# Kernel tuning notes

Measured on AMD Instinct MI355X. Metric: run time of the kernel, lower is better.

The kernel has to match this reference:

```python
import jax, jax.numpy as jnp
import numpy as np

ALPHA = 0.2   # LeakyReLU negative slope
NEG = -1e9    # mask value for non-edges


def setup_inputs() -> dict:
    key = jax.random.key(0)
    ks = jax.random.split(key, 8)
    N, Din, F, H, Dout = 4096, 512, 64, 8, 16
    adj = (jax.random.uniform(ks[0], (N, N)) < 0.01).astype(jnp.float32)
    adjacency = jnp.maximum(adj, jnp.eye(N, dtype=jnp.float32))
    X = jax.random.normal(ks[1], (N, Din), jnp.float32)
    s = lambda k, shape, fan: jax.random.normal(k, shape, jnp.float32) / np.float32(np.sqrt(fan))
    W = s(ks[2], (H, Din, F), Din)        # per-head projection, stacked
    a1 = s(ks[3], (H, F), F)              # attention vector, source half
    a2 = s(ks[4], (H, F), F)              # attention vector, target half
    Wo = s(ks[5], (H * F, Dout), H * F)   # output-layer projection
    ao1 = s(ks[6], (Dout,), Dout)
    ao2 = s(ks[7], (Dout,), Dout)
    return dict(adjacency=adjacency, X=X, W=W, a1=a1, a2=a2, Wo=Wo, ao1=ao1, ao2=ao2)


def reference(adjacency, X, W, a1, a2, Wo, ao1, ao2):
    # dropout is identity (eval mode / p=0)
    mask = adjacency > 0
    N = X.shape[0]
    # --- multi-head attention layers (concat=True -> ELU) ---
    Wh = jnp.einsum('nd,hdf->hnf', X, W)                      # [H, N, F]
    f1 = jnp.einsum('hnf,hf->hn', Wh, a1)                     # [H, N]
    f2 = jnp.einsum('hnf,hf->hn', Wh, a2)                     # [H, N]
    e = jax.nn.leaky_relu(f1[:, :, None] + f2[:, None, :], ALPHA)  # [H, N, N]
    att = jax.nn.softmax(jnp.where(mask[None], e, NEG), axis=-1)
    heads = jax.nn.elu(jnp.einsum('hnm,hmf->hnf', att, Wh))   # [H, N, F]
    cat = jnp.transpose(heads, (1, 0, 2)).reshape(N, -1)      # [N, H*F]
    # --- output attention layer (concat=False -> no ELU) ---
    Who = cat @ Wo                                            # [N, Dout]
    eo = jax.nn.leaky_relu((Who @ ao1)[:, None] + (Who @ ao2)[None, :], ALPHA)
    atto = jax.nn.softmax(jnp.where(mask, eo, NEG), axis=-1)  # [N, N]
    return atto @ Who                                         # [N, Dout]
```

## Files before the change

### kernel.cpp

```cpp
#include <hip/hip_runtime.h>
#include <hip/hip_bf16.h>

#define N_NODES 4096
#define DIN     512
#define FDIM    64
#define NHEADS  8
#define DOUT    16
#define MAXN    512

typedef __attribute__((ext_vector_type(8))) short bf16x8;
typedef __attribute__((ext_vector_type(4))) float f32x4;

static __device__ __forceinline__ float us2f(unsigned short u) {
    union { unsigned int i; float f; } cv; cv.i = ((unsigned int)u) << 16; return cv.f;
}
static __device__ __forceinline__ unsigned short f2us(float v) {
    __hip_bfloat16 b = __float2bfloat16(v);
    return *(const unsigned short*)&b;
}
static __device__ __forceinline__ int is_f32(const void* adj) {
    return (((const unsigned short*)adj)[0] == 0) ? 1 : 0;
}

__global__ __launch_bounds__(256) void prep_kernel(
    const void* __restrict__ adj, const void* __restrict__ W,
    const void* __restrict__ a1, const void* __restrict__ a2, const void* __restrict__ Wo,
    const void* __restrict__ ao1, const void* __restrict__ ao2,
    unsigned short* __restrict__ Wt, float* __restrict__ Woc,
    float* __restrict__ a1c, float* __restrict__ a2c,
    float* __restrict__ ao1c, float* __restrict__ ao2c)
{
    const int f32 = is_f32(adj);
    const int b = blockIdx.x;
    const int t = threadIdx.x;
    if (b < 64) {
        const int h  = b >> 3;
        const int d0 = (b & 7) * 64;
        __shared__ float tile[64][65];
        const size_t wbase = (size_t)h * DIN * FDIM + (size_t)d0 * FDIM;
#pragma unroll
        for (int pass = 0; pass < 16; ++pass) {
            int i = pass * 256 + t;
            int dl = i >> 6, f = i & 63;
            float v = f32 ? ((const float*)W)[wbase + dl * FDIM + f]
                          : us2f(((const unsigned short*)W)[wbase + dl * FDIM + f]);
            tile[dl][f] = v;
        }
        __syncthreads();
#pragma unroll
        for (int pass = 0; pass < 16; ++pass) {
            int i = pass * 256 + t;
            int f = i >> 6, dl = i & 63;
            Wt[((size_t)(h * FDIM + f)) * DIN + d0 + dl] = f2us(tile[dl][f]);
        }
        return;
    }
    const int i0 = (b - 64) * 256 + t;
    for (int i = i0; i < DIN * DOUT; i += 2048) {
        float v = f32 ? ((const float*)Wo)[i] : us2f(((const unsigned short*)Wo)[i]);
        Woc[i] = v;
    }
    if (i0 < 512) {
        a1c[i0] = f32 ? ((const float*)a1)[i0] : us2f(((const unsigned short*)a1)[i0]);
        a2c[i0] = f32 ? ((const float*)a2)[i0] : us2f(((const unsigned short*)a2)[i0]);
    }
    if (i0 < 16) {
        ao1c[i0] = f32 ? ((const float*)ao1)[i0] : us2f(((const unsigned short*)ao1)[i0]);
        ao2c[i0] = f32 ? ((const float*)ao2)[i0] : us2f(((const unsigned short*)ao2)[i0]);
    }
}

__global__ __launch_bounds__(256) void scan_wh_kernel(
    const void* __restrict__ adj, const void* __restrict__ X,
    const unsigned short* __restrict__ Wt,
    const float* __restrict__ a1c, const float* __restrict__ a2c,
    int* __restrict__ cnt, int* __restrict__ nbr,
    unsigned short* __restrict__ Whb, float* __restrict__ f1, float* __restrict__ f2)
{
    const int b   = blockIdx.x;
    const int tid = threadIdx.x;
    const int f32 = is_f32(adj);
    const int wv   = tid >> 6;
    const int lane = tid & 63;

    __shared__ float red[3][16][68];

    if (b < 1024) {
        const int n = b * 4 + wv;
        const unsigned long long lmask = (1ull << lane) - 1ull;
        int c = 0;
        int* nrow = nbr + (size_t)n * MAXN;
        if (f32) {
            const uint4* row = (const uint4*)((const unsigned int*)adj + (size_t)n * N_NODES);
#pragma unroll 4
            for (int it = 0; it < 16; ++it) {
                uint4 v = row[it * 64 + lane];
                int base = (it * 64 + lane) * 4;
                unsigned long long m0 = __ballot(v.x != 0u);
                unsigned long long m1 = __ballot(v.y != 0u);
                unsigned long long m2 = __ballot(v.z != 0u);
                unsigned long long m3 = __ballot(v.w != 0u);
                int p;
                p = c + __popcll(m0 & lmask); if (v.x && p < MAXN) nrow[p] = base + 0; c += __popcll(m0);
                p = c + __popcll(m1 & lmask); if (v.y && p < MAXN) nrow[p] = base + 1; c += __popcll(m1);
                p = c + __popcll(m2 & lmask); if (v.z && p < MAXN) nrow[p] = base + 2; c += __popcll(m2);
                p = c + __popcll(m3 & lmask); if (v.w && p < MAXN) nrow[p] = base + 3; c += __popcll(m3);
            }
        } else {
            const ushort4* row = (const ushort4*)((const unsigned short*)adj + (size_t)n * N_NODES);
#pragma unroll 4
            for (int it = 0; it < 16; ++it) {
                ushort4 v = row[it * 64 + lane];
                int base = (it * 64 + lane) * 4;
                unsigned long long m0 = __ballot(v.x != 0);
                unsigned long long m1 = __ballot(v.y != 0);
                unsigned long long m2 = __ballot(v.z != 0);
                unsigned long long m3 = __ballot(v.w != 0);
                int p;
                p = c + __popcll(m0 & lmask); if (v.x && p < MAXN) nrow[p] = base + 0; c += __popcll(m0);
                p = c + __popcll(m1 & lmask); if (v.y && p < MAXN) nrow[p] = base + 1; c += __popcll(m1);
                p = c + __popcll(m2 & lmask); if (v.z && p < MAXN) nrow[p] = base + 2; c += __popcll(m2);
                p = c + __popcll(m3 & lmask); if (v.w && p < MAXN) nrow[p] = base + 3; c += __popcll(m3);
            }
        }
        if (lane == 0) cnt[n] = (c < MAXN) ? c : MAXN;
        return;
    }

    const int tile = b - 1024;
    const int nt   = tile >> 3;
    const int h    = tile & 7;
    const int quad = lane >> 4;
    const int l16  = lane & 15;
    const int node = nt * 16 + l16;
    const int kbase = wv * 128 + quad * 8;

    f32x4 acc[4];
#pragma unroll
    for (int j = 0; j < 4; ++j) acc[j] = (f32x4){0.f, 0.f, 0.f, 0.f};

    const unsigned short* wp = Wt + (size_t)h * FDIM * DIN + kbase;
    if (f32) {
        const float* xp = (const float*)X + (size_t)node * DIN + kbase;
#pragma unroll
        for (int ks = 0; ks < 4; ++ks) {
            float4 xa = *(const float4*)(xp + ks * 32);
            float4 xb = *(const float4*)(xp + ks * 32 + 4);
            bf16x8 xf;
            xf[0] = (short)f2us(xa.x); xf[1] = (short)f2us(xa.y);
            xf[2] = (short)f2us(xa.z); xf[3] = (short)f2us(xa.w);
            xf[4] = (short)f2us(xb.x); xf[5] = (short)f2us(xb.y);
            xf[6] = (short)f2us(xb.z); xf[7] = (short)f2us(xb.w);
#pragma unroll
            for (int j = 0; j < 4; ++j) {
                bf16x8 wf = *(const bf16x8*)(wp + (size_t)(j * 16 + l16) * DIN + ks * 32);
                acc[j] = __builtin_amdgcn_mfma_f32_16x16x32_bf16(wf, xf, acc[j], 0, 0, 0);
            }
        }
    } else {
        const unsigned short* xp = (const unsigned short*)X + (size_t)node * DIN + kbase;
#pragma unroll
        for (int ks = 0; ks < 4; ++ks) {
            bf16x8 xf = *(const bf16x8*)(xp + ks * 32);
#pragma unroll
            for (int j = 0; j < 4; ++j) {
                bf16x8 wf = *(const bf16x8*)(wp + (size_t)(j * 16 + l16) * DIN + ks * 32);
                acc[j] = __builtin_amdgcn_mfma_f32_16x16x32_bf16(wf, xf, acc[j], 0, 0, 0);
            }
        }
    }

    if (wv) {
#pragma unroll
        for (int j = 0; j < 4; ++j)
            *(f32x4*)&red[wv - 1][l16][j * 16 + quad * 4] = acc[j];
    }
    __syncthreads();
    if (wv == 0) {
        float p1 = 0.f, p2 = 0.f;
#pragma unroll
        for (int j = 0; j < 4; ++j) {
            const int fbase = j * 16 + quad * 4;
            f32x4 s = acc[j];
#pragma unroll
            for (int p = 0; p < 3; ++p) s += *(const f32x4*)&red[p][l16][fbase];
            ushort4 st;
            st.x = f2us(s[0]); st.y = f2us(s[1]);
            st.z = f2us(s[2]); st.w = f2us(s[3]);
            *(ushort4*)&Whb[((size_t)node * NHEADS + h) * FDIM + fbase] = st;
#pragma unroll
            for (int rr = 0; rr < 4; ++rr) {
                p1 += s[rr] * a1c[h * FDIM + fbase + rr];
                p2 += s[rr] * a2c[h * FDIM + fbase + rr];
            }
        }
        p1 += __shfl_xor(p1, 16); p1 += __shfl_xor(p1, 32);
        p2 += __shfl_xor(p2, 16); p2 += __shfl_xor(p2, 32);
        if (quad == 0) {
            f1[h * N_NODES + node] = p1;
            f2[h * N_NODES + node] = p2;
        }
    }
}

__global__ __launch_bounds__(256) void attn1_kernel(
    const unsigned short* __restrict__ Whb,
    const float* __restrict__ f1, const float* __restrict__ f2,
    const float* __restrict__ Woc,
    const float* __restrict__ ao1c, const float* __restrict__ ao2c,
    const int* __restrict__ cnt, const int* __restrict__ nbr,
    float* __restrict__ Who, float* __restrict__ g1, float* __restrict__ g2)
{
    const int n   = blockIdx.x;
    const int tid = threadIdx.x;
    const int wv  = tid >> 6;
    const int lane = tid & 63;
    const int hh = lane >> 3;

    __shared__ int   sh_m[MAXN];
    __shared__ float sh_red[3][64][9];
    __shared__ float sh_ml[4][NHEADS][2];
    __shared__ float cat_sh[512];
    __shared__ float sh_p[16 * 17];

    const int c0 = cnt[n];
    const int c = (c0 < MAXN) ? c0 : MAXN;
    for (int k = tid; k < c; k += 256) sh_m[k] = nbr[(size_t)n * MAXN + k];
    __syncthreads();

    const float f1v = f1[hh * N_NODES + n];
    float m_run = -1e30f, l_run = 0.f;
    float acc8[8];
#pragma unroll
    for (int e = 0; e < 8; ++e) acc8[e] = 0.f;
    const uint4* wb = (const uint4*)Whb;
#pragma unroll 2
    for (int kb = 0; kb < c; kb += 4) {
        const int k = kb + wv;
        if (k < c) {
            const int mm = sh_m[k];
            uint4 v = wb[(size_t)mm * 64 + lane];
            float s = f1v + f2[hh * N_NODES + mm];
            s = (s >= 0.f) ? s : 0.2f * s;
            if (s > m_run + 8.f) {
                float scale = __expf(m_run - s);
                l_run *= scale;
#pragma unroll
                for (int e = 0; e < 8; ++e) acc8[e] *= scale;
                m_run = s;
            }
            float wgt = __expf(s - m_run);
            l_run += wgt;
            acc8[0] += wgt * us2f((unsigned short)(v.x & 0xFFFFu));
            acc8[1] += wgt * us2f((unsigned short)(v.x >> 16));
            acc8[2] += wgt * us2f((unsigned short)(v.y & 0xFFFFu));
            acc8[3] += wgt * us2f((unsigned short)(v.y >> 16));
            acc8[4] += wgt * us2f((unsigned short)(v.z & 0xFFFFu));
            acc8[5] += wgt * us2f((unsigned short)(v.z >> 16));
            acc8[6] += wgt * us2f((unsigned short)(v.w & 0xFFFFu));
            acc8[7] += wgt * us2f((unsigned short)(v.w >> 16));
        }
    }
    if (wv) {
#pragma unroll
        for (int e = 0; e < 8; ++e) sh_red[wv - 1][lane][e] = acc8[e];
    }
    if ((lane & 7) == 0) {
        sh_ml[wv][hh][0] = m_run;
        sh_ml[wv][hh][1] = l_run;
    }
    __syncthreads();
    if (wv == 0) {
        float m1 = sh_ml[1][hh][0], m2 = sh_ml[2][hh][0], m3 = sh_ml[3][hh][0];
        float M = fmaxf(fmaxf(m_run, m1), fmaxf(m2, m3));
        float c0f = __expf(m_run - M), c1f = __expf(m1 - M);
        float c2f = __expf(m2 - M),  c3f = __expf(m3 - M);
        float denom = l_run * c0f + sh_ml[1][hh][1] * c1f
                    + sh_ml[2][hh][1] * c2f + sh_ml[3][hh][1] * c3f;
        const float inv = (denom > 0.f) ? 1.f / denom : 0.f;
#pragma unroll
        for (int e = 0; e < 8; ++e) {
            float s = acc8[e] * c0f + sh_red[0][lane][e] * c1f
                    + sh_red[1][lane][e] * c2f + sh_red[2][lane][e] * c3f;
            s *= inv;
            s = (s > 0.f) ? s : expm1f(s);
            cat_sh[lane * 8 + e] = s;
        }
    }
    __syncthreads();

    {
        const int j = tid & 15, ch = tid >> 4;
        float s = 0.f;
#pragma unroll
        for (int d = 0; d < 32; ++d)
            s += cat_sh[ch * 32 + d] * Woc[(ch * 32 + d) * DOUT + j];
        sh_p[ch * 17 + j] = s;
    }
    __syncthreads();
    if (tid < 16) {
        float s = 0.f;
#pragma unroll
        for (int ch = 0; ch < 16; ++ch) s += sh_p[ch * 17 + tid];
        Who[n * DOUT + tid] = s;
        float p1 = s * ao1c[tid];
        float p2 = s * ao2c[tid];
#pragma unroll
        for (int off = 8; off; off >>= 1) {
            p1 += __shfl_xor(p1, off);
            p2 += __shfl_xor(p2, off);
        }
        if (tid == 0) { g1[n] = p1; g2[n] = p2; }
    }
}

__global__ __launch_bounds__(256) void attn2_kernel(
    const void* __restrict__ adj,
    const float* __restrict__ Who,
    const float* __restrict__ g1, const float* __restrict__ g2,
    const int* __restrict__ cnt, const int* __restrict__ nbr,
    void* __restrict__ out)
{
    const int wv   = threadIdx.x >> 6;
    const int lane = threadIdx.x & 63;
    const int n = blockIdx.x * 4 + wv;
    const int quad = lane >> 4, l16 = lane & 15;
    __shared__ float sh_s[4][MAXN];
    __shared__ int   sh_m[4][MAXN];
    const int c0 = cnt[n];
    const int c = (c0 < MAXN) ? c0 : MAXN;
    for (int k = lane; k < c; k += 64) sh_m[wv][k] = nbr[(size_t)n * MAXN + k];
    const float gn = g1[n];
    float mx = -1e30f;
    for (int k = lane; k < c; k += 64) {
        float s = gn + g2[sh_m[wv][k]];
        s = (s >= 0.f) ? s : 0.2f * s;
        sh_s[wv][k] = s;
        mx = fmaxf(mx, s);
    }
#pragma unroll
    for (int off = 32; off; off >>= 1) mx = fmaxf(mx, __shfl_xor(mx, off));
    float sum = 0.f;
    for (int k = lane; k < c; k += 64) {
        float e = __expf(sh_s[wv][k] - mx);
        sh_s[wv][k] = e;
        sum += e;
    }
#pragma unroll
    for (int off = 32; off; off >>= 1) sum += __shfl_xor(sum, off);
    const float inv = (sum > 0.f) ? 1.f / sum : 0.f;
    float accv = 0.f;
#pragma unroll 4
    for (int k = quad; k < c; k += 4)
        accv += sh_s[wv][k] * Who[sh_m[wv][k] * DOUT + l16];
    accv += __shfl_xor(accv, 16);
    accv += __shfl_xor(accv, 32);
    if (quad == 0) {
        float v = accv * inv;
        if (is_f32(adj)) ((float*)out)[n * DOUT + l16] = v;
        else             ((unsigned short*)out)[n * DOUT + l16] = f2us(v);
    }
}

__global__ void wsfail_kernel(float* __restrict__ out)
{
    if (threadIdx.x == 0) out[0] = 129.f;
}

extern "C" void kernel_launch(void* const* d_in, const int* in_sizes, int n_in,
                              void* d_out, int out_size, void* d_ws, size_t ws_size,
                              hipStream_t stream)
{
    const void* adj = d_in[0];
    const void* X   = d_in[1];
    const void* W   = d_in[2];
    const void* a1  = d_in[3];
    const void* a2  = d_in[4];
    const void* Wo  = d_in[5];
    const void* ao1 = d_in[6];
    const void* ao2 = d_in[7];

    const size_t NEEDED = 22000000;
    if (ws_size < NEEDED) { wsfail_kernel<<<1, 64, 0, stream>>>((float*)d_out); return; }

    int*   cnt  = (int*)d_ws;
    int*   nbr  = cnt + 4096;
    float* a1c  = (float*)(nbr + 2097152);
    float* a2c  = a1c + 512;
    float* ao1c = a2c + 512;
    float* ao2c = ao1c + 16;
    float* f1   = ao2c + 16;
    float* f2   = f1 + 32768;
    float* Who  = f2 + 32768;
    float* g1   = Who + 65536;
    float* g2   = g1 + 4096;
    float* Woc  = g2 + 4096;
    unsigned short* Whb = (unsigned short*)(Woc + 8192);
    unsigned short* Wt  = Whb + 2097152;

    prep_kernel<<<72, 256, 0, stream>>>(
        adj, W, a1, a2, Wo, ao1, ao2, Wt, Woc, a1c, a2c, ao1c, ao2c);
    scan_wh_kernel<<<3072, 256, 0, stream>>>(
        adj, X, Wt, a1c, a2c, cnt, nbr, Whb, f1, f2);
    attn1_kernel<<<N_NODES, 256, 0, stream>>>(
        Whb, f1, f2, Woc, ao1c, ao2c, cnt, nbr, Who, g1, g2);
    attn2_kernel<<<N_NODES / 4, 256, 0, stream>>>(adj, Who, g1, g2, cnt, nbr, d_out);
}
```

Baseline: 168.0 us.

## Interleave adjacency-scan and projection blocks; split row scans into atomic chunks

Odd and even blocks of the combined kernel now alternate between adjacency scanning and the X·W projection tiles. The memory-bound scan and the compute-bound GEMM can then run on the GPU at the same time instead of the scan blocks all running first. The scan is also reorganised: each wave processes 1KB chunks in a grid-stride loop and reserves slots in the per-row neighbour list with an atomicAdd on cnt, which prep_kernel now zeroes. Neighbour order becomes nondeterministic, and cnt is no longer clamped to MAXN, so rows with more than 512 neighbours could overflow what downstream kernels expect.

```diff
diff --git a/kernel.cpp b/kernel.cpp
--- a/kernel.cpp
+++ b/kernel.cpp
@@ -28,7 +28,8 @@
     const void* __restrict__ ao1, const void* __restrict__ ao2,
     unsigned short* __restrict__ Wt, float* __restrict__ Woc,
     float* __restrict__ a1c, float* __restrict__ a2c,
-    float* __restrict__ ao1c, float* __restrict__ ao2c)
+    float* __restrict__ ao1c, float* __restrict__ ao2c,
+    int* __restrict__ cnt)
 {
     const int f32 = is_f32(adj);
     const int b = blockIdx.x;
@@ -56,6 +57,8 @@
         return;
     }
     const int i0 = (b - 64) * 256 + t;
+    cnt[i0] = 0;
+    cnt[i0 + 2048] = 0;
     for (int i = i0; i < DIN * DOUT; i += 2048) {
         float v = f32 ? ((const float*)Wo)[i] : us2f(((const unsigned short*)Wo)[i]);
         Woc[i] = v;
@@ -70,7 +73,7 @@
     }
 }
 
-__global__ __launch_bounds__(256) void scan_wh_kernel(
+__global__ __launch_bounds__(256) void scanwh_kernel(
     const void* __restrict__ adj, const void* __restrict__ X,
     const unsigned short* __restrict__ Wt,
     const float* __restrict__ a1c, const float* __restrict__ a2c,
@@ -85,49 +88,74 @@
 
     __shared__ float red[3][16][68];
 
-    if (b < 1024) {
-        const int n = b * 4 + wv;
+    if (b & 1) {
         const unsigned long long lmask = (1ull << lane) - 1ull;
-        int c = 0;
-        int* nrow = nbr + (size_t)n * MAXN;
+        const int sid = (b >> 1) * 4 + wv;
+        const uint4* a4 = (const uint4*)adj;
         if (f32) {
-            const uint4* row = (const uint4*)((const unsigned int*)adj + (size_t)n * N_NODES);
-#pragma unroll 4
-            for (int it = 0; it < 16; ++it) {
-                uint4 v = row[it * 64 + lane];
-                int base = (it * 64 + lane) * 4;
+            const int NCH = (N_NODES * (N_NODES / 256));
+#pragma unroll 2
+            for (int chunk = sid; chunk < NCH; chunk += 8192) {
+                const int row = chunk >> 4;
+                uint4 v = a4[(size_t)chunk * 64 + lane];
                 unsigned long long m0 = __ballot(v.x != 0u);
                 unsigned long long m1 = __ballot(v.y != 0u);
                 unsigned long long m2 = __ballot(v.z != 0u);
                 unsigned long long m3 = __ballot(v.w != 0u);
-                int p;
-                p = c + __popcll(m0 & lmask); if (v.x && p < MAXN) nrow[p] = base + 0; c += __popcll(m0);
-                p = c + __popcll(m1 & lmask); if (v.y && p < MAXN) nrow[p] = base + 1; c += __popcll(m1);
-                p = c + __popcll(m2 & lmask); if (v.z && p < MAXN) nrow[p] = base + 2; c += __popcll(m2);
-                p = c + __popcll(m3 & lmask); if (v.w && p < MAXN) nrow[p] = base + 3; c += __popcll(m3);
+                int c0 = __popcll(m0), c1 = __popcll(m1), c2 = __popcll(m2), c3 = __popcll(m3);
+                int tot = c0 + c1 + c2 + c3;
+                if (tot) {
+                    int base;
+                    if (lane == 0) base = atomicAdd(&cnt[row], tot);
+                    base = __shfl(base, 0);
+                    int* nrow = nbr + (size_t)row * MAXN;
+                    const int eb = (chunk & 15) * 256 + lane * 4;
+                    int p;
+                    p = base + __popcll(m0 & lmask);                 if (v.x && p < MAXN) nrow[p] = eb + 0;
+                    p = base + c0 + __popcll(m1 & lmask);            if (v.y && p < MAXN) nrow[p] = eb + 1;
+                    p = base + c0 + c1 + __popcll(m2 & lmask);       if (v.z && p < MAXN) nrow[p] = eb + 2;
+                    p = base + c0 + c1 + c2 + __popcll(m3 & lmask);  if (v.w && p < MAXN) nrow[p] = eb + 3;
+                }
             }
         } else {
-            const ushort4* row = (const ushort4*)((const unsigned short*)adj + (size_t)n * N_NODES);
-#pragma unroll 4
-            for (int it = 0; it < 16; ++it) {
-                ushort4 v = row[it * 64 + lane];
-                int base = (it * 64 + lane) * 4;
-                unsigned long long m0 = __ballot(v.x != 0);
-                unsigned long long m1 = __ballot(v.y != 0);
-                unsigned long long m2 = __ballot(v.z != 0);
-                unsigned long long m3 = __ballot(v.w != 0);
-                int p;
-                p = c + __popcll(m0 & lmask); if (v.x && p < MAXN) nrow[p] = base + 0; c += __popcll(m0);
-                p = c + __popcll(m1 & lmask); if (v.y && p < MAXN) nrow[p] = base + 1; c += __popcll(m1);
-                p = c + __popcll(m2 & lmask); if (v.z && p < MAXN) nrow[p] = base + 2; c += __popcll(m2);
-                p = c + __popcll(m3 & lmask); if (v.w && p < MAXN) nrow[p] = base + 3; c += __popcll(m3);
-            }
-        }
-        if (lane == 0) cnt[n] = (c < MAXN) ? c : MAXN;
+            const int NCH = (N_NODES * (N_NODES / 512));
+#pragma unroll 2
+            for (int chunk = sid; chunk < NCH; chunk += 8192) {
+                const int row = chunk >> 3;
+                uint4 v = a4[(size_t)chunk * 64 + lane];
+                unsigned short e0 = (unsigned short)(v.x & 0xFFFFu), e1 = (unsigned short)(v.x >> 16);
+                unsigned short e2 = (unsigned short)(v.y & 0xFFFFu), e3 = (unsigned short)(v.y >> 16);
+                unsigned short e4 = (unsigned short)(v.z & 0xFFFFu), e5 = (unsigned short)(v.z >> 16);
+                unsigned short e6 = (unsigned short)(v.w & 0xFFFFu), e7 = (unsigned short)(v.w >> 16);
+                unsigned long long m0 = __ballot(e0 != 0), m1 = __ballot(e1 != 0);
+                unsigned long long m2 = __ballot(e2 != 0), m3 = __ballot(e3 != 0);
+                unsigned long long m4 = __ballot(e4 != 0), m5 = __ballot(e5 != 0);
+                unsigned long long m6 = __ballot(e6 != 0), m7 = __ballot(e7 != 0);
+                int c0=__popcll(m0), c1=__popcll(m1), c2=__popcll(m2), c3=__popcll(m3);
+                int c4=__popcll(m4), c5=__popcll(m5), c6=__popcll(m6), c7=__popcll(m7);
+                int tot = c0+c1+c2+c3+c4+c5+c6+c7;
+                if (tot) {
+                    int base;
+                    if (lane == 0) base = atomicAdd(&cnt[row], tot);
+                    base = __shfl(base, 0);
+                    int* nrow = nbr + (size_t)row * MAXN;
+                    const int eb = (chunk & 7) * 512 + lane * 8;
+                    int s = base, p;
+                    p = s + __popcll(m0 & lmask); if (e0 && p < MAXN) nrow[p] = eb + 0; s += c0;
+                    p = s + __popcll(m1 & lmask); if (e1 && p < MAXN) nrow[p] = eb + 1; s += c1;
+                    p = s + __popcll(m2 & lmask); if (e2 && p < MAXN) nrow[p] = eb + 2; s += c2;
+                    p = s + __popcll(m3 & lmask); if (e3 && p < MAXN) nrow[p] = eb + 3; s += c3;
+                    p = s + __popcll(m4 & lmask); if (e4 && p < MAXN) nrow[p] = eb + 4; s += c4;
+                    p = s + __popcll(m5 & lmask); if (e5 && p < MAXN) nrow[p] = eb + 5; s += c5;
+                    p = s + __popcll(m6 & lmask); if (e6 && p < MAXN) nrow[p] = eb + 6; s += c6;
+                    p = s + __popcll(m7 & lmask); if (e7 && p < MAXN) nrow[p] = eb + 7;
+                }
+            }
+        }
         return;
     }
 
-    const int tile = b - 1024;
+    const int tile = b >> 1;
     const int nt   = tile >> 3;
     const int h    = tile & 7;
     const int quad = lane >> 4;
@@ -399,8 +427,8 @@
     unsigned short* Wt  = Whb + 2097152;
 
     prep_kernel<<<72, 256, 0, stream>>>(
-        adj, W, a1, a2, Wo, ao1, ao2, Wt, Woc, a1c, a2c, ao1c, ao2c);
-    scan_wh_kernel<<<3072, 256, 0, stream>>>(
+        adj, W, a1, a2, Wo, ao1, ao2, Wt, Woc, a1c, a2c, ao1c, ao2c, cnt);
+    scanwh_kernel<<<4096, 256, 0, stream>>>(
         adj, X, Wt, a1c, a2c, cnt, nbr, Whb, f1, f2);
     attn1_kernel<<<N_NODES, 256, 0, stream>>>(
         Whb, f1, f2, Woc, ao1c, ao2c, cnt, nbr, Who, g1, g2);
```

Result: slower. 187.5 us (+11.6%).
